# Performance work log

Measured on AMD Instinct MI355X. Metric: run time of the kernel, lower is better.

## Reference

```python
import jax, jax.numpy as jnp
import numpy as np

B, L, D, K = 16, 2048, 768, 32
NEG = jnp.float32(-1e30)

def setup_inputs() -> dict:
    key = jax.random.key(0)
    k1, k2, k3, k4 = jax.random.split(key, 4)
    token_hidden = jax.random.normal(k1, (B, L, D), dtype=jnp.float32)
    attention_mask = jnp.ones((B, L), dtype=jnp.float32)
    # ragged spans: sorted boundaries -> contiguous, possibly-empty spans
    bounds = jnp.sort(jax.random.randint(k2, (B, K + 1), 0, L), axis=-1)
    span_starts = bounds[:, :-1].astype(jnp.int32)   # [B, K]
    span_ends = bounds[:, 1:].astype(jnp.int32)      # [B, K]
    w_pool = jax.random.normal(k3, (D,), dtype=jnp.float32) * 0.02
    b_pool = jax.random.normal(k4, (1,), dtype=jnp.float32) * 0.02
    return {"token_hidden": token_hidden, "attention_mask": attention_mask,
            "span_starts": span_starts, "span_ends": span_ends,
            "w_pool": w_pool, "b_pool": b_pool}

def reference(token_hidden, attention_mask, span_starts, span_ends, w_pool, b_pool):
    # sent_pool(vecs): scores per token, shared across spans  -> [B, L]
    scores = jnp.einsum('bld,d->bl', token_hidden, w_pool) + b_pool[0]
    pos = jnp.arange(token_hidden.shape[1], dtype=jnp.int32)  # [L]
    # span membership mask [B, K, L]; empty / out-of-range spans -> all False
    span_mask = ((pos[None, None, :] >= span_starts[:, :, None]) &
                 (pos[None, None, :] < span_ends[:, :, None]) &
                 (attention_mask[:, None, :] >= 0.5))
    logits = jnp.where(span_mask, scores[:, None, :], NEG)  # [B, K, L]
    m = jnp.max(logits, axis=-1, keepdims=True)
    e = jnp.exp(logits - m) * span_mask                      # stable masked softmax
    s = jnp.sum(e, axis=-1, keepdims=True)
    w = e / jnp.maximum(s, jnp.float32(1e-30))               # zero rows for empty spans
    H = jnp.einsum('bkl,bld->bkd', w, token_hidden)          # [B, K, D]
    sent_mask = jnp.any(span_mask, axis=-1).astype(jnp.float32)  # [B, K]
    return H, sent_mask
```

## Files before the change

kernel.cpp:

```cpp
#include <hip/hip_runtime.h>

#define BB 16
#define LL 2048
#define DD 768
#define KK 32
#define TILE 32
#define NEGI -1e30f

__global__ __launch_bounds__(256) void scores_k(
    const float* __restrict__ th,
    const float* __restrict__ attn,
    const float* __restrict__ wp,
    const float* __restrict__ bp,
    float* __restrict__ scores,
    float* __restrict__ wbuf,
    int* __restrict__ idbuf) {
  const int lane = threadIdx.x & 63;
  const int wave = threadIdx.x >> 6;
  const int token = (blockIdx.x << 2) + wave;

  const float4* row = (const float4*)(th + (size_t)token * DD);
  const float4* wr  = (const float4*)wp;

  float4 a0 = row[lane], a1 = row[lane + 64], a2 = row[lane + 128];
  float4 w0 = wr[lane],  w1 = wr[lane + 64],  w2 = wr[lane + 128];

  float acc = 0.f;
  acc = fmaf(a0.x, w0.x, acc); acc = fmaf(a0.y, w0.y, acc);
  acc = fmaf(a0.z, w0.z, acc); acc = fmaf(a0.w, w0.w, acc);
  acc = fmaf(a1.x, w1.x, acc); acc = fmaf(a1.y, w1.y, acc);
  acc = fmaf(a1.z, w1.z, acc); acc = fmaf(a1.w, w1.w, acc);
  acc = fmaf(a2.x, w2.x, acc); acc = fmaf(a2.y, w2.y, acc);
  acc = fmaf(a2.z, w2.z, acc); acc = fmaf(a2.w, w2.w, acc);

  #pragma unroll
  for (int o = 32; o > 0; o >>= 1) acc += __shfl_xor(acc, o, 64);

  if (lane == 0) {
    float s = acc + bp[0];
    scores[token] = (attn[token] >= 0.5f) ? s : NEGI;
    wbuf[token]   = 0.f;
    idbuf[token]  = -1;
  }
}

__global__ __launch_bounds__(64) void spanprep_k(
    const int* __restrict__ sps,
    const int* __restrict__ spe,
    const float* __restrict__ scores,
    float* __restrict__ wbuf,
    int* __restrict__ idbuf,
    float* __restrict__ Hout,
    float* __restrict__ sent) {
  const int bk = blockIdx.x;
  const int b = bk >> 5;
  const int k = bk & 31;
  const int lane = threadIdx.x;

  float4* hrow = (float4*)(Hout + (size_t)bk * DD);
  #pragma unroll
  for (int i = lane; i < DD / 4; i += 64) hrow[i] = make_float4(0.f, 0.f, 0.f, 0.f);

  int s0 = min(max(sps[bk], 0), LL);
  int e0 = min(max(spe[bk], 0), LL);

  const float* sc = scores + (size_t)b * LL;

  float m = NEGI;
  for (int l = s0 + lane; l < e0; l += 64) m = fmaxf(m, sc[l]);
  #pragma unroll
  for (int o = 32; o > 0; o >>= 1) m = fmaxf(m, __shfl_xor(m, o, 64));

  float ss = 0.f;
  for (int l = s0 + lane; l < e0; l += 64) {
    float v = sc[l];
    ss += (v > -1e29f) ? __expf(v - m) : 0.f;
  }
  #pragma unroll
  for (int o = 32; o > 0; o >>= 1) ss += __shfl_xor(ss, o, 64);

  const float inv = (ss > 0.f) ? (1.0f / ss) : 0.f;

  for (int l = s0 + lane; l < e0; l += 64) {
    float v = sc[l];
    wbuf[(size_t)b * LL + l] = (v > -1e29f) ? (__expf(v - m) * inv) : 0.f;
    idbuf[(size_t)b * LL + l] = k;
  }

  if (lane == 0) sent[bk] = (ss > 0.f) ? 1.0f : 0.0f;
}

__global__ __launch_bounds__(64) void pool_k(
    const float* __restrict__ th,
    const float* __restrict__ wbuf,
    const int* __restrict__ idbuf,
    float* __restrict__ Hout) {
  const int b = blockIdx.x;
  const int tile0 = blockIdx.y * TILE;
  const int chunk = blockIdx.z;
  const int lane = threadIdx.x;

  __shared__ float lw[TILE];
  __shared__ int lid[TILE];
  if (lane < TILE) {
    lw[lane]  = wbuf[(size_t)b * LL + tile0 + lane];
    lid[lane] = idbuf[(size_t)b * LL + tile0 + lane];
  }
  __syncthreads();

  const float4* base = (const float4*)(th + (size_t)b * LL * DD + chunk * 256) + lane;

  float4 acc = make_float4(0.f, 0.f, 0.f, 0.f);
  int cur = lid[0];

  #pragma unroll 8
  for (int t = 0; t < TILE; ++t) {
    const int id = lid[t];
    const float wt = lw[t];
    if (id != cur) {
      if (cur >= 0) {
        float* o = Hout + ((size_t)(b * KK + cur) * DD) + chunk * 256 + (lane << 2);
        atomicAdd(o + 0, acc.x); atomicAdd(o + 1, acc.y);
        atomicAdd(o + 2, acc.z); atomicAdd(o + 3, acc.w);
      }
      acc = make_float4(0.f, 0.f, 0.f, 0.f);
      cur = id;
    }
    float4 v = base[(size_t)(tile0 + t) * (DD / 4)];
    acc.x = fmaf(wt, v.x, acc.x);
    acc.y = fmaf(wt, v.y, acc.y);
    acc.z = fmaf(wt, v.z, acc.z);
    acc.w = fmaf(wt, v.w, acc.w);
  }
  if (cur >= 0) {
    float* o = Hout + ((size_t)(b * KK + cur) * DD) + chunk * 256 + (lane << 2);
    atomicAdd(o + 0, acc.x); atomicAdd(o + 1, acc.y);
    atomicAdd(o + 2, acc.z); atomicAdd(o + 3, acc.w);
  }
}

extern "C" void kernel_launch(void* const* d_in, const int* in_sizes, int n_in,
                              void* d_out, int out_size, void* d_ws, size_t ws_size,
                              hipStream_t stream) {
  const float* th   = (const float*)d_in[0];
  const float* attn = (const float*)d_in[1];
  const int*   sps  = (const int*)d_in[2];
  const int*   spe  = (const int*)d_in[3];
  const float* wp   = (const float*)d_in[4];
  const float* bp   = (const float*)d_in[5];

  float* Hout = (float*)d_out;
  float* sent = Hout + (size_t)BB * KK * DD;

  float* scores = (float*)d_ws;
  float* wbuf   = scores + (size_t)BB * LL;
  int*   idbuf  = (int*)(wbuf + (size_t)BB * LL);

  scores_k<<<dim3((BB * LL) / 4), dim3(256), 0, stream>>>(
      th, attn, wp, bp, scores, wbuf, idbuf);
  spanprep_k<<<dim3(BB * KK), dim3(64), 0, stream>>>(
      sps, spe, scores, wbuf, idbuf, Hout, sent);
  pool_k<<<dim3(BB, LL / TILE, 3), dim3(64), 0, stream>>>(th, wbuf, idbuf, Hout);
}
```

Measured before the change: 180.8 us.

## Fuse span softmax and pooling into one per-span kernel without atomics

Merges the span-prep and pooling kernels into one kernel launched per (batch, span, chunk). Each block recomputes its span's softmax weights into shared memory and then accumulates the weighted sum over its own tokens, writing the output directly. This drops the wbuf/idbuf buffers, the zero-fill of H, the atomics, and one launch. In exchange, each span's softmax is computed redundantly across the 3 chunks, and ragged span lengths leave the work unevenly balanced across only 1536 small blocks.

```diff
diff --git a/kernel.cpp b/kernel.cpp
--- a/kernel.cpp
+++ b/kernel.cpp
@@ -4,7 +4,6 @@
 #define LL 2048
 #define DD 768
 #define KK 32
-#define TILE 32
 #define NEGI -1e30f
 
 __global__ __launch_bounds__(256) void scores_k(
@@ -12,9 +11,7 @@
     const float* __restrict__ attn,
     const float* __restrict__ wp,
     const float* __restrict__ bp,
-    float* __restrict__ scores,
-    float* __restrict__ wbuf,
-    int* __restrict__ idbuf) {
+    float* __restrict__ scores) {
   const int lane = threadIdx.x & 63;
   const int wave = threadIdx.x >> 6;
   const int token = (blockIdx.x << 2) + wave;
@@ -39,27 +36,22 @@
   if (lane == 0) {
     float s = acc + bp[0];
     scores[token] = (attn[token] >= 0.5f) ? s : NEGI;
-    wbuf[token]   = 0.f;
-    idbuf[token]  = -1;
   }
 }
 
-__global__ __launch_bounds__(64) void spanprep_k(
+__global__ __launch_bounds__(64) void pool2_k(
+    const float* __restrict__ th,
+    const float* __restrict__ scores,
     const int* __restrict__ sps,
     const int* __restrict__ spe,
-    const float* __restrict__ scores,
-    float* __restrict__ wbuf,
-    int* __restrict__ idbuf,
     float* __restrict__ Hout,
     float* __restrict__ sent) {
   const int bk = blockIdx.x;
+  const int chunk = blockIdx.y;
   const int b = bk >> 5;
-  const int k = bk & 31;
   const int lane = threadIdx.x;
 
-  float4* hrow = (float4*)(Hout + (size_t)bk * DD);
-  #pragma unroll
-  for (int i = lane; i < DD / 4; i += 64) hrow[i] = make_float4(0.f, 0.f, 0.f, 0.f);
+  __shared__ float lw[LL];
 
   int s0 = min(max(sps[bk], 0), LL);
   int e0 = min(max(spe[bk], 0), LL);
@@ -83,60 +75,26 @@
 
   for (int l = s0 + lane; l < e0; l += 64) {
     float v = sc[l];
-    wbuf[(size_t)b * LL + l] = (v > -1e29f) ? (__expf(v - m) * inv) : 0.f;
-    idbuf[(size_t)b * LL + l] = k;
-  }
-
-  if (lane == 0) sent[bk] = (ss > 0.f) ? 1.0f : 0.0f;
-}
-
-__global__ __launch_bounds__(64) void pool_k(
-    const float* __restrict__ th,
-    const float* __restrict__ wbuf,
-    const int* __restrict__ idbuf,
-    float* __restrict__ Hout) {
-  const int b = blockIdx.x;
-  const int tile0 = blockIdx.y * TILE;
-  const int chunk = blockIdx.z;
-  const int lane = threadIdx.x;
-
-  __shared__ float lw[TILE];
-  __shared__ int lid[TILE];
-  if (lane < TILE) {
-    lw[lane]  = wbuf[(size_t)b * LL + tile0 + lane];
-    lid[lane] = idbuf[(size_t)b * LL + tile0 + lane];
+    lw[l - s0] = (v > -1e29f) ? (__expf(v - m) * inv) : 0.f;
   }
   __syncthreads();
 
   const float4* base = (const float4*)(th + (size_t)b * LL * DD + chunk * 256) + lane;
+  float4 acc = make_float4(0.f, 0.f, 0.f, 0.f);
+  #pragma unroll 8
+  for (int l = s0; l < e0; ++l) {
+    const float w = lw[l - s0];
+    float4 t = base[(size_t)l * (DD / 4)];
+    acc.x = fmaf(w, t.x, acc.x);
+    acc.y = fmaf(w, t.y, acc.y);
+    acc.z = fmaf(w, t.z, acc.z);
+    acc.w = fmaf(w, t.w, acc.w);
+  }
 
-  float4 acc = make_float4(0.f, 0.f, 0.f, 0.f);
-  int cur = lid[0];
+  float4* o = (float4*)(Hout + (size_t)bk * DD + chunk * 256) + lane;
+  *o = acc;
 
-  #pragma unroll 8
-  for (int t = 0; t < TILE; ++t) {
-    const int id = lid[t];
-    const float wt = lw[t];
-    if (id != cur) {
-      if (cur >= 0) {
-        float* o = Hout + ((size_t)(b * KK + cur) * DD) + chunk * 256 + (lane << 2);
-        atomicAdd(o + 0, acc.x); atomicAdd(o + 1, acc.y);
-        atomicAdd(o + 2, acc.z); atomicAdd(o + 3, acc.w);
-      }
-      acc = make_float4(0.f, 0.f, 0.f, 0.f);
-      cur = id;
-    }
-    float4 v = base[(size_t)(tile0 + t) * (DD / 4)];
-    acc.x = fmaf(wt, v.x, acc.x);
-    acc.y = fmaf(wt, v.y, acc.y);
-    acc.z = fmaf(wt, v.z, acc.z);
-    acc.w = fmaf(wt, v.w, acc.w);
-  }
-  if (cur >= 0) {
-    float* o = Hout + ((size_t)(b * KK + cur) * DD) + chunk * 256 + (lane << 2);
-    atomicAdd(o + 0, acc.x); atomicAdd(o + 1, acc.y);
-    atomicAdd(o + 2, acc.z); atomicAdd(o + 3, acc.w);
-  }
+  if (chunk == 0 && lane == 0) sent[bk] = (ss > 0.f) ? 1.0f : 0.0f;
 }
 
 extern "C" void kernel_launch(void* const* d_in, const int* in_sizes, int n_in,
@@ -153,12 +111,7 @@
   float* sent = Hout + (size_t)BB * KK * DD;
 
   float* scores = (float*)d_ws;
-  float* wbuf   = scores + (size_t)BB * LL;
-  int*   idbuf  = (int*)(wbuf + (size_t)BB * LL);
 
-  scores_k<<<dim3((BB * LL) / 4), dim3(256), 0, stream>>>(
-      th, attn, wp, bp, scores, wbuf, idbuf);
-  spanprep_k<<<dim3(BB * KK), dim3(64), 0, stream>>>(
-      sps, spe, scores, wbuf, idbuf, Hout, sent);
-  pool_k<<<dim3(BB, LL / TILE, 3), dim3(64), 0, stream>>>(th, wbuf, idbuf, Hout);
+  scores_k<<<dim3((BB * LL) / 4), dim3(256), 0, stream>>>(th, attn, wp, bp, scores);
+  pool2_k<<<dim3(BB * KK, 3), dim3(64), 0, stream>>>(th, scores, sps, spe, Hout, sent);
 }
```

After: 174.5 us. 3.5% less time.
